# Kernel tuning notes

Measured on AMD Instinct MI355X. Metric: run time of the kernel, lower is better.

## Reference

```python
import jax, jax.numpy as jnp
import numpy as np

HEADS = 8
DIM_HEAD = 64
DIM = 512
TOP_K = -1  # -1 -> L_context // heads
EPS_LN = 1e-5
EPS_L2 = 1e-12


def chan_ln(x, g):
    # channel LayerNorm over axis 1 of [B, C, H, W], unbiased=False variance
    mean = x.mean(axis=1, keepdims=True)
    var = x.var(axis=1, keepdims=True)
    return (x - mean) * jax.lax.rsqrt(var + EPS_LN) * g[None, :, None, None]


def l2norm(x, axis):
    n = jnp.linalg.norm(x, axis=axis, keepdims=True)
    return x / jnp.maximum(n, EPS_L2)


def conv1x1(x, w):
    # w: [out_c, in_c], x: [B, in_c, H, W]
    return jnp.einsum('oc,bchw->bohw', w, x)


def select_kv(q, k, v, top_k, key):
    # q: [BH, Lq, d]; k, v: [BH, Lkv, d]
    BH, Lq, d = q.shape
    idx_rand = jax.random.randint(key, (BH, top_k), 0, Lq)
    q_small = jnp.take_along_axis(q, idx_rand[:, :, None], axis=1)  # [BH, top_k, d]

    def per(args):
        k_b, qs_b = args  # [Lkv, d], [top_k, d]
        dist = jnp.sum(jnp.abs(k_b[:, None, :] - qs_b[None, :, :]), axis=-1)  # L1 cdist [Lkv, top_k]
        min_dist = dist.min(axis=1)  # [Lkv]
        _, idx = jax.lax.top_k(-min_dist, top_k)  # smallest distances
        return idx

    idx = jax.lax.map(per, (k, q_small))  # [BH, top_k]
    sel_k = jnp.take_along_axis(k, idx[:, :, None], axis=1)
    sel_v = jnp.take_along_axis(v, idx[:, :, None], axis=1)
    return sel_k, sel_v


def setup_inputs() -> dict:
    key = jax.random.key(0)
    ks = jax.random.split(key, 8)
    B, H, W = 8, 48, 48
    inner = HEADS * DIM_HEAD
    return {
        'query_source': jax.random.normal(ks[0], (B, DIM, H, W), jnp.float32),
        'context': jax.random.normal(ks[1], (B, DIM, H, W), jnp.float32),
        'g_ctx': jnp.ones((DIM,), jnp.float32),
        'g_qs': jnp.ones((DIM,), jnp.float32),
        'g_outn': jnp.ones((DIM,), jnp.float32),
        'w_kv': jax.random.normal(ks[2], (2 * inner, DIM), jnp.float32) * (DIM ** -0.5),
        'w_q': jax.random.normal(ks[3], (inner, DIM), jnp.float32) * (DIM ** -0.5),
        'w_out': jax.random.normal(ks[4], (DIM, inner), jnp.float32) * (inner ** -0.5),
        'gamma': jnp.full((1,), 0.5, jnp.float32),
    }


def reference(query_source, context, g_ctx, g_qs, g_outn, w_kv, w_q, w_out, gamma):
    b, c, hq, wq = query_source.shape
    hc, wc = context.shape[2], context.shape[3]
    inner = HEADS * DIM_HEAD

    ctx = chan_ln(context, g_ctx)
    qs = chan_ln(query_source, g_qs)

    kv = conv1x1(ctx, w_kv)            # [b, 2*inner, hc, wc]
    k, v = kv[:, :inner], kv[:, inner:]
    q = conv1x1(qs, w_q)               # [b, inner, hq, wq]

    # fold heads: [b, heads, dim_head, H, W]
    q = q.reshape(b, HEADS, DIM_HEAD, hq, wq)
    k = k.reshape(b, HEADS, DIM_HEAD, hc, wc)
    v = v.reshape(b, HEADS, DIM_HEAD, hc, wc)

    # l2 normalize over the per-head channel dim (original: F.normalize(dim=1) on [(bh), d, H, W])
    q = l2norm(q, axis=2)
    k = l2norm(k, axis=2)

    # flatten spatial: [b, heads, L, d]
    q = q.reshape(b, HEADS, DIM_HEAD, hq * wq).transpose(0, 1, 3, 2)
    k = k.reshape(b, HEADS, DIM_HEAD, hc * wc).transpose(0, 1, 3, 2)
    v = v.reshape(b, HEADS, DIM_HEAD, hc * wc).transpose(0, 1, 3, 2)

    L_ctx = k.shape[2]
    top_k = TOP_K if TOP_K > 0 else L_ctx // HEADS
    if top_k < L_ctx:
        BH = b * HEADS
        sk, sv = select_kv(q.reshape(BH, -1, DIM_HEAD),
                           k.reshape(BH, -1, DIM_HEAD),
                           v.reshape(BH, -1, DIM_HEAD),
                           top_k, jax.random.key(42))
        k = sk.reshape(b, HEADS, top_k, DIM_HEAD)
        v = sv.reshape(b, HEADS, top_k, DIM_HEAD)

    # SDPA with scale=1.0, no mask, eval (dropout 0)
    scores = jnp.einsum('bhqd,bhkd->bhqk', q, k)
    attn = jax.nn.softmax(scores, axis=-1)
    out = jnp.einsum('bhqk,bhkd->bhqd', attn, v)

    # [b, heads, L, d] -> [b, heads*dim_head, hq, wq]
    out = out.transpose(0, 1, 3, 2).reshape(b, inner, hq, wq)
    out = conv1x1(out, w_out)
    out = chan_ln(out, g_outn)
    return gamma * out + query_source
```

## Files before the change

### kernel.cpp

```cpp
#include <hip/hip_runtime.h>
#include <hip/hip_bf16.h>

#define BB 8
#define CC 512
#define LLOC 2304
#define NHEADS 8
#define DH 64
#define BH 64
#define TKSEL 288

typedef unsigned int u32;
typedef short short8 __attribute__((ext_vector_type(8)));
typedef float f32x4 __attribute__((ext_vector_type(4)));
typedef float f32x2 __attribute__((ext_vector_type(2)));

__device__ inline unsigned short f2bf(float f) {
  unsigned u = __float_as_uint(f);
  u += 0x7FFFu + ((u >> 16) & 1u);
  return (unsigned short)(u >> 16);
}
__device__ inline float b2f(unsigned short h) {
  return __uint_as_float(((unsigned)h) << 16);
}

#define GLOAD_LDS(gsrc, ldst) \
  __builtin_amdgcn_global_load_lds((const __attribute__((address_space(1))) u32*)(gsrc), \
                                   (__attribute__((address_space(3))) u32*)(ldst), 16, 0, 0)

__global__ __launch_bounds__(256) void k_ln_stats(const float* __restrict__ x,
                                                  float* __restrict__ st) {
  int b = blockIdx.y;
  int lx = threadIdx.x & 63;
  int cg = threadIdx.x >> 6;
  int loc = blockIdx.x * 64 + lx;
  const float* xb = x + (size_t)b * CC * LLOC;
  float s = 0.f, s2 = 0.f;
  for (int c = cg; c < CC; c += 4) {
    float v = xb[(size_t)c * LLOC + loc];
    s += v; s2 += v * v;
  }
  __shared__ float sh[2][256];
  sh[0][threadIdx.x] = s; sh[1][threadIdx.x] = s2;
  __syncthreads();
  if (threadIdx.x < 64) {
    int t = threadIdx.x;
    float S  = sh[0][t] + sh[0][t+64] + sh[0][t+128] + sh[0][t+192];
    float S2 = sh[1][t] + sh[1][t+64] + sh[1][t+128] + sh[1][t+192];
    float mean = S * (1.f/512.f);
    float var  = S2 * (1.f/512.f) - mean * mean;
    float rstd = 1.f / sqrtf(var + 1e-5f);
    size_t o = ((size_t)b * LLOC + blockIdx.x*64 + t) * 2;
    st[o] = mean; st[o+1] = rstd;
  }
}

__device__ inline void tf2x32(unsigned ks0, unsigned ks1, unsigned x0, unsigned x1,
                              unsigned& y0, unsigned& y1) {
  unsigned ks2 = ks0 ^ ks1 ^ 0x1BD11BDAu;
#define TF_R(r) { x0 += x1; x1 = (x1 << (r)) | (x1 >> (32-(r))); x1 ^= x0; }
  x0 += ks0; x1 += ks1;
  TF_R(13) TF_R(15) TF_R(26) TF_R(6)
  x0 += ks1; x1 += ks2 + 1u;
  TF_R(17) TF_R(29) TF_R(16) TF_R(24)
  x0 += ks2; x1 += ks0 + 2u;
  TF_R(13) TF_R(15) TF_R(26) TF_R(6)
  x0 += ks0; x1 += ks1 + 3u;
  TF_R(17) TF_R(29) TF_R(16) TF_R(24)
  x0 += ks1; x1 += ks2 + 4u;
  TF_R(13) TF_R(15) TF_R(26) TF_R(6)
  x0 += ks2; x1 += ks0 + 5u;
#undef TF_R
  y0 = x0; y1 = x1;
}

__global__ __launch_bounds__(256) void k_threefry(int* __restrict__ idxRand) {
  unsigned i = blockIdx.x * 256 + threadIdx.x;
  if (i >= 18432u) return;
  unsigned a0, a1, b0, b1;
  tf2x32(0u, 42u, 0u, 0u, a0, a1);
  tf2x32(0u, 42u, 0u, 1u, b0, b1);
  unsigned h0, h1, l0, l1;
  tf2x32(a0, a1, 0u, i, h0, h1);
  tf2x32(b0, b1, 0u, i, l0, l1);
  unsigned h = h0 ^ h1;
  unsigned l = l0 ^ l1;
  const unsigned span = 2304u;
  idxRand[i] = (int)(((h % span) * 256u + (l % span)) % span);
}

__global__ __launch_bounds__(256) void k_prep_w(const float* __restrict__ W,
    const float* __restrict__ G, unsigned short* __restrict__ Wh,
    unsigned short* __restrict__ Wl, int total) {
  int i = (blockIdx.x * 256 + threadIdx.x) * 2;
  if (i >= total) return;
  int c = i & 511;
  float2 w2 = *(const float2*)&W[i];
  float g0 = G ? G[c] : 1.f, g1 = G ? G[c+1] : 1.f;
  float f0 = w2.x * g0, f1 = w2.y * g1;
  unsigned short h0 = f2bf(f0), h1 = f2bf(f1);
  unsigned short q0 = f2bf(f0 - b2f(h0)), q1 = f2bf(f1 - b2f(h1));
  *(unsigned*)&Wh[i] = (unsigned)h0 | ((unsigned)h1 << 16);
  *(unsigned*)&Wl[i] = (unsigned)q0 | ((unsigned)q1 << 16);
}

__global__ __launch_bounds__(256) void k_prep_x(const float* __restrict__ X,
    const float* __restrict__ stats, unsigned short* __restrict__ Xh,
    unsigned short* __restrict__ Xl) {
  int b = blockIdx.z, c0 = blockIdx.y * 64, loc0 = blockIdx.x * 64;
  int t = threadIdx.x;
  __shared__ float sm[64][65];
  int lx = t & 63;
  float mean = stats[((size_t)b * LLOC + loc0 + lx) * 2];
  float rstd = stats[((size_t)b * LLOC + loc0 + lx) * 2 + 1];
#pragma unroll
  for (int i = 0; i < 16; ++i) {
    int c = (t >> 6) + i * 4;
    float v = X[((size_t)b * CC + c0 + c) * LLOC + loc0 + lx];
    sm[c][lx] = (v - mean) * rstd;
  }
  __syncthreads();
  int loc = t >> 2, cs = (t & 3) * 16;
  unsigned uh[8], ul[8];
#pragma unroll
  for (int j = 0; j < 8; ++j) {
    float f0 = sm[cs + j*2][loc];
    float f1 = sm[cs + j*2 + 1][loc];
    unsigned short h0 = f2bf(f0), h1 = f2bf(f1);
    unsigned short q0 = f2bf(f0 - b2f(h0)), q1 = f2bf(f1 - b2f(h1));
    uh[j] = (unsigned)h0 | ((unsigned)h1 << 16);
    ul[j] = (unsigned)q0 | ((unsigned)q1 << 16);
  }
  size_t base = ((size_t)b * LLOC + loc0 + loc) * 512 + c0 + cs;
  *(uint4*)(Xh + base)     = make_uint4(uh[0], uh[1], uh[2], uh[3]);
  *(uint4*)(Xh + base + 8) = make_uint4(uh[4], uh[5], uh[6], uh[7]);
  *(uint4*)(Xl + base)     = make_uint4(ul[0], ul[1], ul[2], ul[3]);
  *(uint4*)(Xl + base + 8) = make_uint4(ul[4], ul[5], ul[6], ul[7]);
}

__global__ __launch_bounds__(256) void k_mfma3(
    const unsigned short* __restrict__ Wh, const unsigned short* __restrict__ Wl,
    const unsigned short* __restrict__ Xh, const unsigned short* __restrict__ Xl,
    float* __restrict__ dst, unsigned short* __restrict__ Qb) {
  int b = blockIdx.z;
  int o0 = blockIdx.y * 128, loc0 = blockIdx.x * 128;
  int t = threadIdx.x, l = t & 63, w = t >> 6;
  int wr = w >> 1, wc = w & 1;
  __shared__ unsigned short Ah[128*64], Al[128*64], Bh[128*64], Bl[128*64];
  f32x4 acc[4][4];
#pragma unroll
  for (int i = 0; i < 4; ++i)
#pragma unroll
    for (int j = 0; j < 4; ++j) acc[i][j] = (f32x4){0.f, 0.f, 0.f, 0.f};

  const char* WhC = (const char*)Wh;
  const char* WlC = (const char*)Wl;
  const char* XhC = (const char*)(Xh + (size_t)b * LLOC * 512);
  const char* XlC = (const char*)(Xl + (size_t)b * LLOC * 512);
  int srow = l >> 3;
  int schunk = (l & 7) ^ srow;

  for (int kt = 0; kt < 8; ++kt) {
    int kb = kt * 128;
#pragma unroll
    for (int j = 0; j < 4; ++j) {
      int r = w * 32 + j * 8;
      size_t arow = (size_t)(o0 + r + srow) * 1024 + kb + schunk * 16;
      size_t brow = (size_t)(loc0 + r + srow) * 1024 + kb + schunk * 16;
      GLOAD_LDS(WhC + arow, ((char*)Ah) + r * 128);
      GLOAD_LDS(WlC + arow, ((char*)Al) + r * 128);
      GLOAD_LDS(XhC + brow, ((char*)Bh) + r * 128);
      GLOAD_LDS(XlC + brow, ((char*)Bl) + r * 128);
    }
    __syncthreads();
#pragma unroll
    for (int ks = 0; ks < 2; ++ks) {
      short8 ah[4], al[4], bh[4], bl[4];
#pragma unroll
      for (int ot = 0; ot < 4; ++ot) {
        int row = wr * 64 + ot * 16 + (l & 15);
        int off = row * 128 + ((ks * 4 + (l >> 4)) ^ (row & 7)) * 16;
        ah[ot] = *(const short8*)(((const char*)Ah) + off);
        al[ot] = *(const short8*)(((const char*)Al) + off);
      }
#pragma unroll
      for (int bt = 0; bt < 4; ++bt) {
        int row = wc * 64 + bt * 16 + (l & 15);
        int off = row * 128 + ((ks * 4 + (l >> 4)) ^ (row & 7)) * 16;
        bh[bt] = *(const short8*)(((const char*)Bh) + off);
        bl[bt] = *(const short8*)(((const char*)Bl) + off);
      }
#pragma unroll
      for (int ot = 0; ot < 4; ++ot)
#pragma unroll
        for (int bt = 0; bt < 4; ++bt) {
          acc[ot][bt] = __builtin_amdgcn_mfma_f32_16x16x32_bf16(ah[ot], bh[bt], acc[ot][bt], 0, 0, 0);
          acc[ot][bt] = __builtin_amdgcn_mfma_f32_16x16x32_bf16(ah[ot], bl[bt], acc[ot][bt], 0, 0, 0);
          acc[ot][bt] = __builtin_amdgcn_mfma_f32_16x16x32_bf16(al[ot], bh[bt], acc[ot][bt], 0, 0, 0);
        }
    }
    __syncthreads();
  }
  int head = (o0 >> 6) + wr;
#pragma unroll
  for (int bt = 0; bt < 4; ++bt) {
    float ss = 0.f;
#pragma unroll
    for (int ot = 0; ot < 4; ++ot)
#pragma unroll
      for (int r = 0; r < 4; ++r) ss += acc[ot][bt][r] * acc[ot][bt][r];
    ss += __shfl_xor(ss, 16, 64);
    ss += __shfl_xor(ss, 32, 64);
    float sc = 1.f / fmaxf(sqrtf(ss), 1e-12f);
    int loc = loc0 + wc * 64 + bt * 16 + (l & 15);
    size_t vecbase = (((size_t)(b * NHEADS + head)) * LLOC + loc) * DH;
#pragma unroll
    for (int ot = 0; ot < 4; ++ot)
#pragma unroll
      for (int r = 0; r < 4; ++r) {
        int d = ot * 16 + (l >> 4) * 4 + r;
        float v = acc[ot][bt][r] * sc;
        dst[vecbase + d] = v;
        if (Qb) Qb[vecbase + ((((d >> 3) ^ (loc & 7)) << 3) | (d & 7))] = f2bf(v);
      }
  }
}

__global__ __launch_bounds__(256) void k_mfma1(int mode,
    const unsigned short* __restrict__ W, const unsigned short* __restrict__ X,
    float* __restrict__ outF, unsigned short* __restrict__ outU) {
  int b = blockIdx.z;
  int o0 = blockIdx.y * 128, loc0 = blockIdx.x * 128;
  int t = threadIdx.x, l = t & 63, w = t >> 6;
  int wr = w >> 1, wc = w & 1;
  __shared__ unsigned short Asm[128*64], Bsm[128*64];
  f32x4 acc[4][4];
#pragma unroll
  for (int i = 0; i < 4; ++i)
#pragma unroll
    for (int j = 0; j < 4; ++j) acc[i][j] = (f32x4){0.f, 0.f, 0.f, 0.f};
  const char* Wc = (const char*)W;
  const char* Xc = (const char*)(X + (size_t)b * LLOC * 512);
  int srow = l >> 3;
  int schunk = (l & 7) ^ srow;
  for (int kt = 0; kt < 8; ++kt) {
    int kb = kt * 128;
#pragma unroll
    for (int j = 0; j < 4; ++j) {
      int r = w * 32 + j * 8;
      GLOAD_LDS(Wc + (size_t)(o0 + r + srow) * 1024 + kb + schunk * 16,
                ((char*)Asm) + r * 128);
      GLOAD_LDS(Xc + (size_t)(loc0 + r + srow) * 1024 + kb + schunk * 16,
                ((char*)Bsm) + r * 128);
    }
    __syncthreads();
#pragma unroll
    for (int ks = 0; ks < 2; ++ks) {
      short8 af[4], bf[4];
#pragma unroll
      for (int ot = 0; ot < 4; ++ot) {
        int row = wr * 64 + ot * 16 + (l & 15);
        af[ot] = *(const short8*)(((const char*)Asm) + row * 128 + (((ks*4 + (l>>4)) ^ (row&7)) * 16));
      }
#pragma unroll
      for (int bt = 0; bt < 4; ++bt) {
        int row = wc * 64 + bt * 16 + (l & 15);
        bf[bt] = *(const short8*)(((const char*)Bsm) + row * 128 + (((ks*4 + (l>>4)) ^ (row&7)) * 16));
      }
#pragma unroll
      for (int ot = 0; ot < 4; ++ot)
#pragma unroll
        for (int bt = 0; bt < 4; ++bt)
          acc[ot][bt] = __builtin_amdgcn_mfma_f32_16x16x32_bf16(af[ot], bf[bt], acc[ot][bt], 0, 0, 0);
    }
    __syncthreads();
  }
#pragma unroll
  for (int ot = 0; ot < 4; ++ot) {
    int ob = o0 + wr * 64 + ot * 16 + (l >> 4) * 4;
#pragma unroll
    for (int bt = 0; bt < 4; ++bt) {
      int loc = loc0 + wc * 64 + bt * 16 + (l & 15);
#pragma unroll
      for (int r = 0; r < 4; ++r) {
        int o = ob + r;
        float v = acc[ot][bt][r];
        if (mode == 2)
          outF[((size_t)b * CC + o) * LLOC + loc] = v;
        else
          outU[(((size_t)(b * NHEADS + (o >> 6))) * LLOC + loc) * DH + (o & 63)] = f2bf(v);
      }
    }
  }
}

__global__ __launch_bounds__(256) void k_mindist(const float* __restrict__ K,
    const float* __restrict__ Q, const int* __restrict__ idxRand,
    float* __restrict__ mindP) {
  int chunk = blockIdx.x, row = blockIdx.y, jz = blockIdx.z;
  __shared__ float qs[72][64];
  int t = threadIdx.x;
  int kk = chunk * 256 + t;
  f32x2 kv[32];
  const f32x2* kp = (const f32x2*)&K[((size_t)row * LLOC + kk) * 64];
#pragma unroll
  for (int d = 0; d < 32; ++d) kv[d] = kp[d];
#pragma unroll
  for (int d = 0; d < 32; ++d) asm volatile("" : "+v"(kv[d]));
  for (int e = t; e < 72 * 16; e += 256) {
    int j = e >> 4, t4 = (e & 15) * 4;
    int qi = idxRand[row * TKSEL + jz * 72 + j];
    *(float4*)&qs[j][t4] = *(const float4*)&Q[((size_t)row * LLOC + qi) * 64 + t4];
  }
  __syncthreads();
  float best = 3.402823e38f;
  for (int j = 0; j < 72; ++j) {
    const float4* q4 = (const float4*)&qs[j][0];
    float s0 = 0.f, s1 = 0.f, s2 = 0.f, s3 = 0.f;
#pragma unroll
    for (int d = 0; d < 4; ++d) {
      float4 qa = q4[d], qb = q4[4 + d], qc = q4[8 + d], qd = q4[12 + d];
      f32x2 qa0 = {qa.x, qa.y}, qa1 = {qa.z, qa.w};
      f32x2 qb0 = {qb.x, qb.y}, qb1 = {qb.z, qb.w};
      f32x2 qc0 = {qc.x, qc.y}, qc1 = {qc.z, qc.w};
      f32x2 qd0 = {qd.x, qd.y}, qd1 = {qd.z, qd.w};
      f32x2 a0, a1, b0, b1, c0, c1, e0, e1;
      asm("v_pk_add_f32 %0, %1, %2 neg_lo:[0,1] neg_hi:[0,1]" : "=v"(a0) : "v"(kv[2*d]),      "v"(qa0));
      asm("v_pk_add_f32 %0, %1, %2 neg_lo:[0,1] neg_hi:[0,1]" : "=v"(a1) : "v"(kv[2*d + 1]),  "v"(qa1));
      asm("v_pk_add_f32 %0, %1, %2 neg_lo:[0,1] neg_hi:[0,1]" : "=v"(b0) : "v"(kv[8 + 2*d]),  "v"(qb0));
      asm("v_pk_add_f32 %0, %1, %2 neg_lo:[0,1] neg_hi:[0,1]" : "=v"(b1) : "v"(kv[8 + 2*d + 1]), "v"(qb1));
      asm("v_pk_add_f32 %0, %1, %2 neg_lo:[0,1] neg_hi:[0,1]" : "=v"(c0) : "v"(kv[16 + 2*d]), "v"(qc0));
      asm("v_pk_add_f32 %0, %1, %2 neg_lo:[0,1] neg_hi:[0,1]" : "=v"(c1) : "v"(kv[16 + 2*d + 1]), "v"(qc1));
      asm("v_pk_add_f32 %0, %1, %2 neg_lo:[0,1] neg_hi:[0,1]" : "=v"(e0) : "v"(kv[24 + 2*d]), "v"(qd0));
      asm("v_pk_add_f32 %0, %1, %2 neg_lo:[0,1] neg_hi:[0,1]" : "=v"(e1) : "v"(kv[24 + 2*d + 1]), "v"(qd1));
      asm("v_add_f32 %0, abs(%1), %0" : "+v"(s0) : "v"(a0.x));
      asm("v_add_f32 %0, abs(%1), %0" : "+v"(s0) : "v"(a0.y));
      asm("v_add_f32 %0, abs(%1), %0" : "+v"(s0) : "v"(a1.x));
      asm("v_add_f32 %0, abs(%1), %0" : "+v"(s0) : "v"(a1.y));
      asm("v_add_f32 %0, abs(%1), %0" : "+v"(s1) : "v"(b0.x));
      asm("v_add_f32 %0, abs(%1), %0" : "+v"(s1) : "v"(b0.y));
      asm("v_add_f32 %0, abs(%1), %0" : "+v"(s1) : "v"(b1.x));
      asm("v_add_f32 %0, abs(%1), %0" : "+v"(s1) : "v"(b1.y));
      asm("v_add_f32 %0, abs(%1), %0" : "+v"(s2) : "v"(c0.x));
      asm("v_add_f32 %0, abs(%1), %0" : "+v"(s2) : "v"(c0.y));
      asm("v_add_f32 %0, abs(%1), %0" : "+v"(s2) : "v"(c1.x));
      asm("v_add_f32 %0, abs(%1), %0" : "+v"(s2) : "v"(c1.y));
      asm("v_add_f32 %0, abs(%1), %0" : "+v"(s3) : "v"(e0.x));
      asm("v_add_f32 %0, abs(%1), %0" : "+v"(s3) : "v"(e0.y));
      asm("v_add_f32 %0, abs(%1), %0" : "+v"(s3) : "v"(e1.x));
      asm("v_add_f32 %0, abs(%1), %0" : "+v"(s3) : "v"(e1.y));
    }
    best = fminf(best, (s0 + s1) + (s2 + s3));
  }
  mindP[((size_t)jz * BH + row) * LLOC + kk] = best;
}

__global__ __launch_bounds__(256) void k_select(const float* __restrict__ mindP,
                                                int* __restrict__ sel) {
  int row = blockIdx.y;
  int i = blockIdx.x * 256 + threadIdx.x;
  __shared__ float dd[LLOC];
  const size_t stride = (size_t)BH * LLOC;
  for (int e = threadIdx.x; e < LLOC; e += 256) {
    size_t o = (size_t)row * LLOC + e;
    float m0 = fminf(mindP[o], mindP[o + stride]);
    float m1 = fminf(mindP[o + 2 * stride], mindP[o + 3 * stride]);
    dd[e] = fminf(m0, m1);
  }
  __syncthreads();
  float di = dd[i];
  int rank = 0;
  for (int j = 0; j < LLOC; j += 4) {
    float4 dj = *(const float4*)&dd[j];
    rank += (dj.x < di) || (dj.x == di && (j+0) < i);
    rank += (dj.y < di) || (dj.y == di && (j+1) < i);
    rank += (dj.z < di) || (dj.z == di && (j+2) < i);
    rank += (dj.w < di) || (dj.w == di && (j+3) < i);
  }
  if (rank < TKSEL) sel[row * TKSEL + rank] = i;
}

__global__ __launch_bounds__(256) void k_gather(const float* __restrict__ K,
    const unsigned short* __restrict__ Vb, const int* __restrict__ sel,
    unsigned short* __restrict__ Kc, unsigned short* __restrict__ Vt) {
  int row = blockIdx.x;
  int d = threadIdx.x & 63;
  for (int ki = threadIdx.x >> 6; ki < TKSEL; ki += 4) {
    int k = sel[row * TKSEL + ki];
    float kv = K[((size_t)row * LLOC + k) * 64 + d];
    Kc[((size_t)row * TKSEL + ki) * 64 + (((d >> 3) ^ (ki & 7)) << 3) + (d & 7)] = f2bf(kv);
    Vt[((size_t)row * 64 + d) * TKSEL + ki] = Vb[((size_t)row * LLOC + k) * 64 + d];
  }
}

__global__ __launch_bounds__(256) void k_attn_mfma(
    const unsigned short* __restrict__ Qb, const unsigned short* __restrict__ Kc,
    const unsigned short* __restrict__ Vt, unsigned short* __restrict__ AOb) {
  int row = blockIdx.y, q0 = blockIdx.x * 64;
  int t = threadIdx.x, l = t & 63, w = t >> 6;
  int q15 = l & 15, l4 = l >> 4;
  __shared__ unsigned short Qsm[64 * 64];
  __shared__ unsigned short Ksm[96 * 64];
  __shared__ unsigned short Vsm[64 * 120];
  __shared__ unsigned short Psm[4 * 512];

  f32x4 oacc[4];
#pragma unroll
  for (int dt = 0; dt < 4; ++dt) oacc[dt] = (f32x4){0.f, 0.f, 0.f, 0.f};
  float lsum = 0.f;

  const char* QbC = (const char*)(Qb + ((size_t)row * LLOC + q0) * 64);
#pragma unroll
  for (int i = 0; i < 2; ++i)
    GLOAD_LDS(QbC + (size_t)(i * 256 + w * 64 + l) * 16, ((char*)Qsm) + (i * 256 + w * 64) * 16);

  for (int c = 0; c < 3; ++c) {
    const char* KcC = (const char*)(Kc + (((size_t)row * TKSEL) + c * 96) * 64);
#pragma unroll
    for (int i = 0; i < 3; ++i)
      GLOAD_LDS(KcC + (size_t)(i * 256 + w * 64 + l) * 16, ((char*)Ksm) + (i * 256 + w * 64) * 16);
#pragma unroll
    for (int i = 0; i < 3; ++i) {
      int s = i * 256 + t;
      int d = s / 12, j = s % 12;
      uint4 v = *(const uint4*)(Vt + ((size_t)row * 64 + d) * TKSEL + c * 96 + j * 8);
      *(uint4*)((char*)Vsm + d * 240 + j * 16) = v;
    }
    __syncthreads();

    f32x4 sacc[6];
#pragma unroll
    for (int kt = 0; kt < 6; ++kt) sacc[kt] = (f32x4){0.f, 0.f, 0.f, 0.f};
#pragma unroll
    for (int ks = 0; ks < 2; ++ks) {
      int qrow = w * 16 + q15;
      short8 qf = *(const short8*)(Qsm + qrow * 64 + (((ks * 4 + l4) ^ (qrow & 7)) << 3));
#pragma unroll
      for (int kt = 0; kt < 6; ++kt) {
        int krow = kt * 16 + q15;
        short8 kf = *(const short8*)(Ksm + krow * 64 + (((ks * 4 + l4) ^ (krow & 7)) << 3));
        sacc[kt] = __builtin_amdgcn_mfma_f32_16x16x32_bf16(kf, qf, sacc[kt], 0, 0, 0);
      }
    }

    char* Pw = (char*)(Psm + w * 512);
#pragma unroll
    for (int s3 = 0; s3 < 3; ++s3) {
#pragma unroll
      for (int h2 = 0; h2 < 2; ++h2) {
        int kt = 2 * s3 + h2;
        float p0 = expf(sacc[kt][0]), p1 = expf(sacc[kt][1]);
        float p2 = expf(sacc[kt][2]), p3 = expf(sacc[kt][3]);
        lsum += (p0 + p1) + (p2 + p3);
        unsigned lo = (unsigned)f2bf(p0) | ((unsigned)f2bf(p1) << 16);
        unsigned hi = (unsigned)f2bf(p2) | ((unsigned)f2bf(p3) << 16);
        int sl = (h2 * 4 + l4) ^ ((q15 & 3) << 1);
        *(uint2*)(Pw + q15 * 64 + sl * 8) = make_uint2(lo, hi);
      }
      short8 pB = *(const short8*)(Pw + q15 * 64 + (((2 * l4) ^ ((q15 & 3) << 1)) * 8));
#pragma unroll
      for (int dt = 0; dt < 4; ++dt) {
        short8 vA = *(const short8*)(Vsm + (dt * 16 + q15) * 120 + s3 * 32 + l4 * 8);
        oacc[dt] = __builtin_amdgcn_mfma_f32_16x16x32_bf16(vA, pB, oacc[dt], 0, 0, 0);
      }
    }
    __syncthreads();
  }

  lsum += __shfl_xor(lsum, 16, 64);
  lsum += __shfl_xor(lsum, 32, 64);
  float inv = 1.f / lsum;
  int bq = row >> 3, hq = row & 7;
  int loc = q0 + w * 16 + q15;
  unsigned short* op = AOb + ((size_t)bq * LLOC + loc) * 512 + hq * 64;
#pragma unroll
  for (int dt = 0; dt < 4; ++dt) {
    unsigned w0 = (unsigned)f2bf(oacc[dt][0] * inv) | ((unsigned)f2bf(oacc[dt][1] * inv) << 16);
    unsigned w1 = (unsigned)f2bf(oacc[dt][2] * inv) | ((unsigned)f2bf(oacc[dt][3] * inv) << 16);
    *(uint2*)(op + dt * 16 + l4 * 4) = make_uint2(w0, w1);
  }
}

__global__ __launch_bounds__(256) void k_final(const float* __restrict__ CO,
    const float* __restrict__ st, const float* __restrict__ g,
    const float* __restrict__ gamma, const float* __restrict__ qsrc,
    float* __restrict__ out) {
  size_t i = (size_t)blockIdx.x * 256 + threadIdx.x;
  int loc = (int)(i % LLOC);
  int c = (int)((i / LLOC) % CC);
  int b = (int)(i / ((size_t)LLOC * CC));
  float mean = st[((size_t)b * LLOC + loc) * 2];
  float rstd = st[((size_t)b * LLOC + loc) * 2 + 1];
  float v = (CO[i] - mean) * rstd * g[c];
  out[i] = gamma[0] * v + qsrc[i];
}

extern "C" void kernel_launch(void* const* d_in, const int* in_sizes, int n_in,
                              void* d_out, int out_size, void* d_ws, size_t ws_size,
                              hipStream_t stream) {
  const float* qsrc  = (const float*)d_in[0];
  const float* ctx   = (const float*)d_in[1];
  const float* g_ctx = (const float*)d_in[2];
  const float* g_qs  = (const float*)d_in[3];
  const float* g_out = (const float*)d_in[4];
  const float* w_kv  = (const float*)d_in[5];
  const float* w_q   = (const float*)d_in[6];
  const float* w_out = (const float*)d_in[7];
  const float* gamma = (const float*)d_in[8];
  float* out = (float*)d_out;

  float* ws = (float*)d_ws;
  float* statsCtx = ws;
  float* statsQs  = ws + 36864;
  int*   idxRand  = (int*)(ws + 73728);
  int*   sel      = (int*)(ws + 92160);
  float* Q  = ws + 258048;
  float* K  = Q + 9437184;
  unsigned short* usb = (unsigned short*)(K + 9437184);
  unsigned short* Vb     = usb;
  unsigned short* Xt_hi  = Vb + 9437184;
  unsigned short* Xt_lo  = Xt_hi + 9437184;
  unsigned short* Wkv_hi = Xt_lo + 9437184;
  unsigned short* Wkv_lo = Wkv_hi + 524288;
  unsigned short* Wq_hi  = Wkv_lo + 524288;
  unsigned short* Wq_lo  = Wq_hi + 262144;
  unsigned short* Wo_hi  = Wq_lo + 262144;
  unsigned short* Wo_lo  = Wo_hi + 262144;
  float* mindP = (float*)(Wo_lo + 262144);
  unsigned short* Kc = (unsigned short*)(mindP + 589824);
  unsigned short* Vt = Kc + 1179648;
  unsigned short* Qb = Vt + 1179648;
  float* CO = Q;

  k_ln_stats<<<dim3(36, 8), 256, 0, stream>>>(ctx, statsCtx);
  k_ln_stats<<<dim3(36, 8), 256, 0, stream>>>(qsrc, statsQs);
  k_threefry<<<72, 256, 0, stream>>>(idxRand);
  k_prep_w<<<1024, 256, 0, stream>>>(w_kv, g_ctx, Wkv_hi, Wkv_lo, 1024 * 512);
  k_prep_w<<<512, 256, 0, stream>>>(w_q, g_qs, Wq_hi, Wq_lo, 512 * 512);
  k_prep_w<<<512, 256, 0, stream>>>(w_out, nullptr, Wo_hi, Wo_lo, 512 * 512);
  k_prep_x<<<dim3(36, 8, 8), 256, 0, stream>>>(ctx, statsCtx, Xt_hi, Xt_lo);
  k_mfma3<<<dim3(18, 4, 8), 256, 0, stream>>>(Wkv_hi, Wkv_lo, Xt_hi, Xt_lo, K, nullptr);
  k_mfma1<<<dim3(18, 4, 8), 256, 0, stream>>>(3, Wkv_hi + 512*512, Xt_hi, nullptr, Vb);
  k_prep_x<<<dim3(36, 8, 8), 256, 0, stream>>>(qsrc, statsQs, Xt_hi, Xt_lo);
  k_mfma3<<<dim3(18, 4, 8), 256, 0, stream>>>(Wq_hi, Wq_lo, Xt_hi, Xt_lo, Q, Qb);
  k_mindist<<<dim3(9, 64, 4), 256, 0, stream>>>(K, Q, idxRand, mindP);
  k_select<<<dim3(9, 64), 256, 0, stream>>>(mindP, sel);
  k_gather<<<64, 256, 0, stream>>>(K, Vb, sel, Kc, Vt);
  k_attn_mfma<<<dim3(36, 64), 256, 0, stream>>>(Qb, Kc, Vt, Xt_hi);
  k_mfma1<<<dim3(18, 4, 8), 256, 0, stream>>>(2, Wo_hi, Xt_hi, CO, nullptr);
  k_ln_stats<<<dim3(36, 8), 256, 0, stream>>>(CO, statsCtx);
  k_final<<<36864, 256, 0, stream>>>(CO, statsCtx, g_out, gamma, qsrc, out);
}
```

Measured before the change: 637.4 us.

## Fuse LayerNorm statistics into prep and final kernels; merge weight prep launches

Computes channel LayerNorm mean/rstd inside the input-prep and final-output kernels instead of separate stats kernels, and merges three weight-prep launches into one. This removes four launches and the stats round trip through global memory. In exchange, the fused kernels launch only 288 blocks each, far fewer than before, which may under-occupy the GPU for these memory-bound passes. Each fused kernel also reads its input twice, though the second read may hit cache.

```diff
diff --git a/kernel.cpp b/kernel.cpp
--- a/kernel.cpp
+++ b/kernel.cpp
@@ -26,33 +26,6 @@
 #define GLOAD_LDS(gsrc, ldst) \
   __builtin_amdgcn_global_load_lds((const __attribute__((address_space(1))) u32*)(gsrc), \
                                    (__attribute__((address_space(3))) u32*)(ldst), 16, 0, 0)
-
-__global__ __launch_bounds__(256) void k_ln_stats(const float* __restrict__ x,
-                                                  float* __restrict__ st) {
-  int b = blockIdx.y;
-  int lx = threadIdx.x & 63;
-  int cg = threadIdx.x >> 6;
-  int loc = blockIdx.x * 64 + lx;
-  const float* xb = x + (size_t)b * CC * LLOC;
-  float s = 0.f, s2 = 0.f;
-  for (int c = cg; c < CC; c += 4) {
-    float v = xb[(size_t)c * LLOC + loc];
-    s += v; s2 += v * v;
-  }
-  __shared__ float sh[2][256];
-  sh[0][threadIdx.x] = s; sh[1][threadIdx.x] = s2;
-  __syncthreads();
-  if (threadIdx.x < 64) {
-    int t = threadIdx.x;
-    float S  = sh[0][t] + sh[0][t+64] + sh[0][t+128] + sh[0][t+192];
-    float S2 = sh[1][t] + sh[1][t+64] + sh[1][t+128] + sh[1][t+192];
-    float mean = S * (1.f/512.f);
-    float var  = S2 * (1.f/512.f) - mean * mean;
-    float rstd = 1.f / sqrtf(var + 1e-5f);
-    size_t o = ((size_t)b * LLOC + blockIdx.x*64 + t) * 2;
-    st[o] = mean; st[o+1] = rstd;
-  }
-}
 
 __device__ inline void tf2x32(unsigned ks0, unsigned ks1, unsigned x0, unsigned x1,
                               unsigned& y0, unsigned& y1) {
@@ -88,14 +61,23 @@
   idxRand[i] = (int)(((h % span) * 256u + (l % span)) % span);
 }
 
-__global__ __launch_bounds__(256) void k_prep_w(const float* __restrict__ W,
-    const float* __restrict__ G, unsigned short* __restrict__ Wh,
-    unsigned short* __restrict__ Wl, int total) {
-  int i = (blockIdx.x * 256 + threadIdx.x) * 2;
-  if (i >= total) return;
+__global__ __launch_bounds__(256) void k_prep_w_all(
+    const float* __restrict__ w_kv, const float* __restrict__ w_q,
+    const float* __restrict__ w_out, const float* __restrict__ g_ctx,
+    const float* __restrict__ g_qs,
+    unsigned short* __restrict__ Wkv_hi, unsigned short* __restrict__ Wkv_lo,
+    unsigned short* __restrict__ Wq_hi,  unsigned short* __restrict__ Wq_lo,
+    unsigned short* __restrict__ Wo_hi,  unsigned short* __restrict__ Wo_lo) {
+  int i2 = (blockIdx.x * 256 + threadIdx.x) * 2;
+  const float* W; const float* G;
+  unsigned short *Wh, *Wl; int base;
+  if (i2 < 524288) { W = w_kv; G = g_ctx; Wh = Wkv_hi; Wl = Wkv_lo; base = 0; }
+  else if (i2 < 786432) { W = w_q; G = g_qs; Wh = Wq_hi; Wl = Wq_lo; base = 524288; }
+  else { W = w_out; G = nullptr; Wh = Wo_hi; Wl = Wo_lo; base = 786432; }
+  int i = i2 - base;
   int c = i & 511;
   float2 w2 = *(const float2*)&W[i];
-  float g0 = G ? G[c] : 1.f, g1 = G ? G[c+1] : 1.f;
+  float g0 = G ? G[c] : 1.f, g1 = G ? G[c + 1] : 1.f;
   float f0 = w2.x * g0, f1 = w2.y * g1;
   unsigned short h0 = f2bf(f0), h1 = f2bf(f1);
   unsigned short q0 = f2bf(f0 - b2f(h0)), q1 = f2bf(f1 - b2f(h1));
@@ -103,38 +85,58 @@
   *(unsigned*)&Wl[i] = (unsigned)q0 | ((unsigned)q1 << 16);
 }
 
-__global__ __launch_bounds__(256) void k_prep_x(const float* __restrict__ X,
-    const float* __restrict__ stats, unsigned short* __restrict__ Xh,
-    unsigned short* __restrict__ Xl) {
-  int b = blockIdx.z, c0 = blockIdx.y * 64, loc0 = blockIdx.x * 64;
-  int t = threadIdx.x;
+__global__ __launch_bounds__(256) void k_prep_xf(const float* __restrict__ X,
+    unsigned short* __restrict__ Xh, unsigned short* __restrict__ Xl) {
+  int b = blockIdx.y, loc0 = blockIdx.x * 64;
+  int t = threadIdx.x, lx = t & 63, cg = t >> 6;
+  const float* xb = X + (size_t)b * CC * LLOC;
+  float s = 0.f, s2 = 0.f;
+  for (int c = cg; c < CC; c += 4) {
+    float v = xb[(size_t)c * LLOC + loc0 + lx];
+    s += v; s2 += v * v;
+  }
+  __shared__ float sh[2][256];
+  __shared__ float mS[64], rS[64];
+  sh[0][t] = s; sh[1][t] = s2;
+  __syncthreads();
+  if (t < 64) {
+    float S  = sh[0][t] + sh[0][t+64] + sh[0][t+128] + sh[0][t+192];
+    float S2 = sh[1][t] + sh[1][t+64] + sh[1][t+128] + sh[1][t+192];
+    float mean = S * (1.f/512.f);
+    float var  = S2 * (1.f/512.f) - mean * mean;
+    mS[t] = mean;
+    rS[t] = 1.f / sqrtf(var + 1e-5f);
+  }
+  __syncthreads();
   __shared__ float sm[64][65];
-  int lx = t & 63;
-  float mean = stats[((size_t)b * LLOC + loc0 + lx) * 2];
-  float rstd = stats[((size_t)b * LLOC + loc0 + lx) * 2 + 1];
-#pragma unroll
-  for (int i = 0; i < 16; ++i) {
-    int c = (t >> 6) + i * 4;
-    float v = X[((size_t)b * CC + c0 + c) * LLOC + loc0 + lx];
-    sm[c][lx] = (v - mean) * rstd;
-  }
-  __syncthreads();
+  float mean = mS[lx], rstd = rS[lx];
   int loc = t >> 2, cs = (t & 3) * 16;
-  unsigned uh[8], ul[8];
-#pragma unroll
-  for (int j = 0; j < 8; ++j) {
-    float f0 = sm[cs + j*2][loc];
-    float f1 = sm[cs + j*2 + 1][loc];
-    unsigned short h0 = f2bf(f0), h1 = f2bf(f1);
-    unsigned short q0 = f2bf(f0 - b2f(h0)), q1 = f2bf(f1 - b2f(h1));
-    uh[j] = (unsigned)h0 | ((unsigned)h1 << 16);
-    ul[j] = (unsigned)q0 | ((unsigned)q1 << 16);
-  }
-  size_t base = ((size_t)b * LLOC + loc0 + loc) * 512 + c0 + cs;
-  *(uint4*)(Xh + base)     = make_uint4(uh[0], uh[1], uh[2], uh[3]);
-  *(uint4*)(Xh + base + 8) = make_uint4(uh[4], uh[5], uh[6], uh[7]);
-  *(uint4*)(Xl + base)     = make_uint4(ul[0], ul[1], ul[2], ul[3]);
-  *(uint4*)(Xl + base + 8) = make_uint4(ul[4], ul[5], ul[6], ul[7]);
+  for (int cc = 0; cc < 8; ++cc) {
+    int c0 = cc * 64;
+#pragma unroll
+    for (int i = 0; i < 16; ++i) {
+      int c = cg + i * 4;
+      float v = xb[(size_t)(c0 + c) * LLOC + loc0 + lx];
+      sm[c][lx] = (v - mean) * rstd;
+    }
+    __syncthreads();
+    unsigned uh[8], ul[8];
+#pragma unroll
+    for (int j = 0; j < 8; ++j) {
+      float f0 = sm[cs + j*2][loc];
+      float f1 = sm[cs + j*2 + 1][loc];
+      unsigned short h0 = f2bf(f0), h1 = f2bf(f1);
+      unsigned short q0 = f2bf(f0 - b2f(h0)), q1 = f2bf(f1 - b2f(h1));
+      uh[j] = (unsigned)h0 | ((unsigned)h1 << 16);
+      ul[j] = (unsigned)q0 | ((unsigned)q1 << 16);
+    }
+    size_t base = ((size_t)b * LLOC + loc0 + loc) * 512 + c0 + cs;
+    *(uint4*)(Xh + base)     = make_uint4(uh[0], uh[1], uh[2], uh[3]);
+    *(uint4*)(Xh + base + 8) = make_uint4(uh[4], uh[5], uh[6], uh[7]);
+    *(uint4*)(Xl + base)     = make_uint4(ul[0], ul[1], ul[2], ul[3]);
+    *(uint4*)(Xl + base + 8) = make_uint4(ul[4], ul[5], ul[6], ul[7]);
+    __syncthreads();
+  }
 }
 
 __global__ __launch_bounds__(256) void k_mfma3(
@@ -480,18 +482,38 @@
   }
 }
 
-__global__ __launch_bounds__(256) void k_final(const float* __restrict__ CO,
-    const float* __restrict__ st, const float* __restrict__ g,
-    const float* __restrict__ gamma, const float* __restrict__ qsrc,
-    float* __restrict__ out) {
-  size_t i = (size_t)blockIdx.x * 256 + threadIdx.x;
-  int loc = (int)(i % LLOC);
-  int c = (int)((i / LLOC) % CC);
-  int b = (int)(i / ((size_t)LLOC * CC));
-  float mean = st[((size_t)b * LLOC + loc) * 2];
-  float rstd = st[((size_t)b * LLOC + loc) * 2 + 1];
-  float v = (CO[i] - mean) * rstd * g[c];
-  out[i] = gamma[0] * v + qsrc[i];
+__global__ __launch_bounds__(256) void k_final_f(const float* __restrict__ CO,
+    const float* __restrict__ g, const float* __restrict__ gamma,
+    const float* __restrict__ qsrc, float* __restrict__ out) {
+  int b = blockIdx.y, loc0 = blockIdx.x * 64;
+  int t = threadIdx.x, lx = t & 63, cg = t >> 6;
+  const float* cb = CO + (size_t)b * CC * LLOC;
+  float s = 0.f, s2 = 0.f;
+  for (int c = cg; c < CC; c += 4) {
+    float v = cb[(size_t)c * LLOC + loc0 + lx];
+    s += v; s2 += v * v;
+  }
+  __shared__ float sh[2][256];
+  __shared__ float mS[64], rS[64];
+  sh[0][t] = s; sh[1][t] = s2;
+  __syncthreads();
+  if (t < 64) {
+    float S  = sh[0][t] + sh[0][t+64] + sh[0][t+128] + sh[0][t+192];
+    float S2 = sh[1][t] + sh[1][t+64] + sh[1][t+128] + sh[1][t+192];
+    float mean = S * (1.f/512.f);
+    float var  = S2 * (1.f/512.f) - mean * mean;
+    mS[t] = mean;
+    rS[t] = 1.f / sqrtf(var + 1e-5f);
+  }
+  __syncthreads();
+  float mean = mS[lx], rstd = rS[lx];
+  float ga = gamma[0];
+  size_t bbase = (size_t)b * CC * LLOC;
+  for (int c = cg; c < CC; c += 4) {
+    size_t off = (size_t)c * LLOC + loc0 + lx;
+    float v = cb[off];
+    out[bbase + off] = ga * (v - mean) * rstd * g[c] + qsrc[bbase + off];
+  }
 }
 
 extern "C" void kernel_launch(void* const* d_in, const int* in_sizes, int n_in,
@@ -509,8 +531,6 @@
   float* out = (float*)d_out;
 
   float* ws = (float*)d_ws;
-  float* statsCtx = ws;
-  float* statsQs  = ws + 36864;
   int*   idxRand  = (int*)(ws + 73728);
   int*   sel      = (int*)(ws + 92160);
   float* Q  = ws + 258048;
@@ -531,22 +551,18 @@
   unsigned short* Qb = Vt + 1179648;
   float* CO = Q;
 
-  k_ln_stats<<<dim3(36, 8), 256, 0, stream>>>(ctx, statsCtx);
-  k_ln_stats<<<dim3(36, 8), 256, 0, stream>>>(qsrc, statsQs);
   k_threefry<<<72, 256, 0, stream>>>(idxRand);
-  k_prep_w<<<1024, 256, 0, stream>>>(w_kv, g_ctx, Wkv_hi, Wkv_lo, 1024 * 512);
-  k_prep_w<<<512, 256, 0, stream>>>(w_q, g_qs, Wq_hi, Wq_lo, 512 * 512);
-  k_prep_w<<<512, 256, 0, stream>>>(w_out, nullptr, Wo_hi, Wo_lo, 512 * 512);
-  k_prep_x<<<dim3(36, 8, 8), 256, 0, stream>>>(ctx, statsCtx, Xt_hi, Xt_lo);
+  k_prep_w_all<<<2048, 256, 0, stream>>>(w_kv, w_q, w_out, g_ctx, g_qs,
+                                         Wkv_hi, Wkv_lo, Wq_hi, Wq_lo, Wo_hi, Wo_lo);
+  k_prep_xf<<<dim3(36, 8), 256, 0, stream>>>(ctx, Xt_hi, Xt_lo);
   k_mfma3<<<dim3(18, 4, 8), 256, 0, stream>>>(Wkv_hi, Wkv_lo, Xt_hi, Xt_lo, K, nullptr);
   k_mfma1<<<dim3(18, 4, 8), 256, 0, stream>>>(3, Wkv_hi + 512*512, Xt_hi, nullptr, Vb);
-  k_prep_x<<<dim3(36, 8, 8), 256, 0, stream>>>(qsrc, statsQs, Xt_hi, Xt_lo);
+  k_prep_xf<<<dim3(36, 8), 256, 0, stream>>>(qsrc, Xt_hi, Xt_lo);
   k_mfma3<<<dim3(18, 4, 8), 256, 0, stream>>>(Wq_hi, Wq_lo, Xt_hi, Xt_lo, Q, Qb);
   k_mindist<<<dim3(9, 64, 4), 256, 0, stream>>>(K, Q, idxRand, mindP);
   k_select<<<dim3(9, 64), 256, 0, stream>>>(mindP, sel);
   k_gather<<<64, 256, 0, stream>>>(K, Vb, sel, Kc, Vt);
   k_attn_mfma<<<dim3(36, 64), 256, 0, stream>>>(Qb, Kc, Vt, Xt_hi);
   k_mfma1<<<dim3(18, 4, 8), 256, 0, stream>>>(2, Wo_hi, Xt_hi, CO, nullptr);
-  k_ln_stats<<<dim3(36, 8), 256, 0, stream>>>(CO, statsCtx);
-  k_final<<<36864, 256, 0, stream>>>(CO, statsCtx, g_out, gamma, qsrc, out);
-}
+  k_final_f<<<dim3(36, 8), 256, 0, stream>>>(CO, g_out, gamma, qsrc, out);
+}
```

Result: no change. 647.5 us (+1.6%).
